# Optimization experiments

Hardware: AMD Instinct MI355X
Metric: run time of the kernel (lower is better)

## Reference

```python
import jax, jax.numpy as jnp
import numpy as np

N = 100000      # nodes
E = 3200000     # edges (avg degree 32)
DIN, DH, DOUT = 128, 32, 2


def setup_inputs() -> dict:
    key = jax.random.key(0)
    k1, k2, k3, k4 = jax.random.split(key, 4)
    x = jax.random.normal(k1, (N, DIN), dtype=jnp.float32)
    edge_index = jax.random.randint(k2, (2, E), 0, N, dtype=jnp.int64)
    # Glorot-ish scaled weights
    W1 = jax.random.normal(k3, (DIN, DH), dtype=jnp.float32) / np.sqrt(DIN)
    b1 = jnp.zeros((DH,), dtype=jnp.float32)
    W2 = jax.random.normal(k4, (DH, DOUT), dtype=jnp.float32) / np.sqrt(DH)
    b2 = jnp.zeros((DOUT,), dtype=jnp.float32)
    return {"x": x, "edge_index": edge_index, "W1": W1, "b1": b1, "W2": W2, "b2": b2}


def reference(x, edge_index, W1, b1, W2, b2):
    n = x.shape[0]
    # GCNConv default: add self-loops, symmetric deg^{-1/2} A deg^{-1/2} normalization
    loops = jnp.arange(n, dtype=edge_index.dtype)
    src = jnp.concatenate([edge_index[0], loops])  # [E+N]
    dst = jnp.concatenate([edge_index[1], loops])  # [E+N]
    deg = jax.ops.segment_sum(jnp.ones_like(dst, dtype=x.dtype), dst, num_segments=n)
    dinv = jnp.where(deg > 0, jax.lax.rsqrt(deg), 0.0)
    norm = dinv[src] * dinv[dst]  # [E+N]

    def gcn_layer(h, W, b):
        m = h @ W                                   # [n, dout] transform first (PyG order)
        msgs = m[src] * norm[:, None]               # gather + scale  [E+N, dout]
        agg = jax.ops.segment_sum(msgs, dst, num_segments=n)  # scatter-add
        return agg + b

    h = jax.nn.relu(gcn_layer(x, W1, b1))
    return gcn_layer(h, W2, b2)
```

## Files before the change

### kernel.cpp

```cpp
#include <hip/hip_runtime.h>
#include <hip/hip_bf16.h>

#define DIN 128
#define DH 32
#define DOUT 2
#define NPB 128
#define NPB_SHIFT 7
#define NBUK_MAX 1024
#define FILL_EDGES 8192

#define FXS1 262144.0f
#define FXI1 (1.0f / 262144.0f)
#define FXS2 131072.0f
#define FXI2 (1.0f / 131072.0f)


__device__ inline unsigned short f2bf(float f) {
    unsigned int u = __float_as_uint(f);
    u = (u + 0x7FFFu + ((u >> 16) & 1u)) >> 16;
    return (unsigned short)u;
}
__device__ inline float bfLO(unsigned int w) { return __uint_as_float(w << 16); }
__device__ inline float bfHI(unsigned int w) { return __uint_as_float(w & 0xFFFF0000u); }

__global__ void zero_gcnt_kernel(int* __restrict__ gcnt, int nbuk) {
    int i = blockIdx.x * blockDim.x + threadIdx.x;
    if (i < nbuk) gcnt[i] = 0;
}

__global__ void bukhist_kernel(const int* __restrict__ dst, int* __restrict__ gcnt,
                               int e, int nbuk) {
    __shared__ int lcnt[NBUK_MAX];
    int t = threadIdx.x;
    for (int i = t; i < nbuk; i += 256) lcnt[i] = 0;
    __syncthreads();
    int e0 = blockIdx.x * FILL_EDGES;
    int m = min(FILL_EDGES, e - e0);
    for (int i = t; i < m; i += 256) atomicAdd(&lcnt[dst[e0 + i] >> NPB_SHIFT], 1);
    __syncthreads();
    for (int i = t; i < nbuk; i += 256)
        if (lcnt[i]) atomicAdd(&gcnt[i], lcnt[i]);
}

__global__ void scan_kernel(const int* __restrict__ gcnt, int* __restrict__ gbase,
                            int* __restrict__ gcur, int nbuk,
                            unsigned short* __restrict__ mqc, int n) {
    __shared__ int sd[256];
    int t = threadIdx.x;
    if (t < 16) ((unsigned int*)(mqc + (size_t)n * DH))[t] = 0u;
    int v[4], s = 0;
#pragma unroll
    for (int k = 0; k < 4; ++k) {
        int i = 4 * t + k;
        v[k] = (i < nbuk) ? gcnt[i] : 0;
        s += v[k];
    }
    sd[t] = s;
    __syncthreads();
    for (int off = 1; off < 256; off <<= 1) {
        int x = (t >= off) ? sd[t - off] : 0;
        __syncthreads();
        sd[t] += x;
        __syncthreads();
    }
    int run = sd[t] - s;
#pragma unroll
    for (int k = 0; k < 4; ++k) {
        int i = 4 * t + k;
        if (i < nbuk) { gbase[i] = run; gcur[i] = run; }
        run += v[k];
    }
}

__global__ void binfill_kernel(const int* __restrict__ src, const int* __restrict__ dst,
                               int* __restrict__ gcur, unsigned int* __restrict__ binned,
                               int e, int nbuk) {
    __shared__ int cnt[NBUK_MAX];
    __shared__ int pos[NBUK_MAX];
    __shared__ int gb[NBUK_MAX];
    __shared__ unsigned int sorted[FILL_EDGES];
    __shared__ unsigned short aux[FILL_EDGES];
    __shared__ int stmp[256];

    int t = threadIdx.x;
    int e0 = blockIdx.x * FILL_EDGES;
    int m = min(FILL_EDGES, e - e0);

    for (int i = t; i < nbuk; i += 256) cnt[i] = 0;
    __syncthreads();
    for (int i = t; i < m; i += 256) atomicAdd(&cnt[dst[e0 + i] >> NPB_SHIFT], 1);
    __syncthreads();

    int v[4], s = 0;
#pragma unroll
    for (int k = 0; k < 4; ++k) {
        int i = 4 * t + k;
        v[k] = (i < nbuk) ? cnt[i] : 0;
        s += v[k];
    }
    stmp[t] = s;
    __syncthreads();
    for (int off = 1; off < 256; off <<= 1) {
        int x = (t >= off) ? stmp[t - off] : 0;
        __syncthreads();
        stmp[t] += x;
        __syncthreads();
    }
    int run = stmp[t] - s;
#pragma unroll
    for (int k = 0; k < 4; ++k) {
        int i = 4 * t + k;
        if (i < nbuk) pos[i] = run;
        run += v[k];
    }
    __syncthreads();

    for (int i = t; i < m; i += 256) {
        int d = dst[e0 + i];
        int sv = src[e0 + i];
        int b = d >> NPB_SHIFT;
        int r = atomicAdd(&pos[b], 1);
        sorted[r] = ((unsigned int)(d & (NPB - 1)) << 17) | (unsigned int)sv;
        aux[r] = (unsigned short)b;
    }
    __syncthreads();

    for (int b = t; b < nbuk; b += 256) {
        int c = cnt[b];
        gb[b] = c ? atomicAdd(&gcur[b], c) : 0;
    }
    __syncthreads();

    for (int i = t; i < m; i += 256) {
        int b = aux[i];
        int start = pos[b] - cnt[b];
        binned[gb[b] + (i - start)] = sorted[i];
    }
}

__global__ void bdinv_kernel(const int* __restrict__ gbase, const int* __restrict__ gcnt,
                             const unsigned int* __restrict__ binned,
                             float* __restrict__ dinv, int n) {
    __shared__ int cnt[NPB];
    int t = threadIdx.x;
    int b = blockIdx.x;
    if (t < NPB) cnt[t] = 0;
    __syncthreads();
    const int beg = gbase[b];
    const int cntb = gcnt[b];
    for (int i = t; i < cntb; i += 256) atomicAdd(&cnt[binned[beg + i] >> 17], 1);
    __syncthreads();
    if (t < NPB) {
        int r = (b << NPB_SHIFT) + t;
        if (r < n) dinv[r] = rsqrtf((float)(cnt[t] + 1));
    }
}

#define XLD 132
__global__ void gemm1_kernel(const float* __restrict__ x, const float* __restrict__ W1,
                             const float* __restrict__ dinv,
                             unsigned short* __restrict__ mqc, int n) {
    __shared__ float  Xl[32 * XLD];
    __shared__ float4 Wl4[DIN * 8];

    int t = threadIdx.x;
    for (int i = t; i < DIN * 8; i += 256) Wl4[i] = ((const float4*)W1)[i];

    int rb = blockIdx.x * 32;
    for (int i = t; i < 32 * 32; i += 256) {
        int rr = i >> 5, c4 = i & 31;
        int gr = rb + rr;
        float4 v = make_float4(0.f, 0.f, 0.f, 0.f);
        if (gr < n) v = ((const float4*)x)[(size_t)gr * 32 + c4];
        ((float4*)Xl)[rr * 33 + c4] = v;
    }
    __syncthreads();

    const int lane = t & 7;
    const int row  = t >> 3;
    const float* xrow = &Xl[row * XLD];
    float4 acc = make_float4(0.f, 0.f, 0.f, 0.f);
#pragma unroll
    for (int k = 0; k < DIN; ++k) {
        float xv = xrow[k];
        float4 w = Wl4[k * 8 + lane];
        acc.x += xv * w.x; acc.y += xv * w.y;
        acc.z += xv * w.z; acc.w += xv * w.w;
    }
    int r = rb + row;
    if (r < n) {
        float di = dinv[r];
        ushort4 sv;
        sv.x = f2bf(acc.x * di); sv.y = f2bf(acc.y * di);
        sv.z = f2bf(acc.z * di); sv.w = f2bf(acc.w * di);
        *(ushort4*)&mqc[(size_t)r * DH + 4 * lane] = sv;
    }
}

__global__ void __launch_bounds__(256, 4)
agg1_kernel(const int* __restrict__ gbase, const int* __restrict__ gcnt,
            const unsigned int* __restrict__ binned,
            const unsigned short* __restrict__ mqc,
            const float* __restrict__ dinv,
            const float* __restrict__ b1, const float* __restrict__ W2,
            float2* __restrict__ m2q, int n) {
    __shared__ int acc[NPB * 33];

    const int t = threadIdx.x;
    const int b = blockIdx.x;
    const int beg = gbase[b];
    const int cntb = gcnt[b];
    const int r0 = b << NPB_SHIFT;

    for (int i = t; i < NPB * 33; i += 256) acc[i] = 0;
    __syncthreads();

    const int g = t >> 4, l = t & 15;
    const unsigned int* __restrict__ bp = binned + beg;
    const unsigned int* __restrict__ mq32 = (const unsigned int*)mqc;

    int i = g;
    for (; i + 48 < cntb; i += 64) {
        unsigned int e0 = __builtin_nontemporal_load(&bp[i]);
        unsigned int e1 = __builtin_nontemporal_load(&bp[i + 16]);
        unsigned int e2 = __builtin_nontemporal_load(&bp[i + 32]);
        unsigned int e3 = __builtin_nontemporal_load(&bp[i + 48]);
        unsigned int w0 = mq32[(e0 & 0x1FFFFu) * 16u + l];
        unsigned int w1 = mq32[(e1 & 0x1FFFFu) * 16u + l];
        unsigned int w2 = mq32[(e2 & 0x1FFFFu) * 16u + l];
        unsigned int w3 = mq32[(e3 & 0x1FFFFu) * 16u + l];
        int d0 = (int)(e0 >> 17) * 33 + 2 * l;
        int d1 = (int)(e1 >> 17) * 33 + 2 * l;
        int d2 = (int)(e2 >> 17) * 33 + 2 * l;
        int d3 = (int)(e3 >> 17) * 33 + 2 * l;
        atomicAdd(&acc[d0], __float2int_rn(bfLO(w0) * FXS1));
        atomicAdd(&acc[d0 + 1], __float2int_rn(bfHI(w0) * FXS1));
        atomicAdd(&acc[d1], __float2int_rn(bfLO(w1) * FXS1));
        atomicAdd(&acc[d1 + 1], __float2int_rn(bfHI(w1) * FXS1));
        atomicAdd(&acc[d2], __float2int_rn(bfLO(w2) * FXS1));
        atomicAdd(&acc[d2 + 1], __float2int_rn(bfHI(w2) * FXS1));
        atomicAdd(&acc[d3], __float2int_rn(bfLO(w3) * FXS1));
        atomicAdd(&acc[d3 + 1], __float2int_rn(bfHI(w3) * FXS1));
    }
    for (; i < cntb; i += 16) {
        unsigned int e0 = __builtin_nontemporal_load(&bp[i]);
        unsigned int w0 = mq32[(e0 & 0x1FFFFu) * 16u + l];
        int d0 = (int)(e0 >> 17) * 33 + 2 * l;
        atomicAdd(&acc[d0], __float2int_rn(bfLO(w0) * FXS1));
        atomicAdd(&acc[d0 + 1], __float2int_rn(bfHI(w0) * FXS1));
    }
    __syncthreads();

    const int j = t >> 1, hf = t & 1;
    const int r = r0 + j;
    if (r < n) {
        const float di = dinv[r];
        const unsigned int* srow = mq32 + (size_t)r * 16 + hf * 8;
        const int* ar = &acc[j * 33 + hf * 16];
        float p0 = 0.f, p1 = 0.f;
#pragma unroll
        for (int k = 0; k < 8; ++k) {
            unsigned int sw = srow[k];
            int c = hf * 16 + 2 * k;
            float a0 = (float)ar[2 * k]     * FXI1;
            float a1 = (float)ar[2 * k + 1] * FXI1;
            float h0 = fmaxf(di * (a0 + bfLO(sw)) + b1[c],     0.0f);
            float h1 = fmaxf(di * (a1 + bfHI(sw)) + b1[c + 1], 0.0f);
            p0 += h0 * W2[2 * c]     + h1 * W2[2 * c + 2];
            p1 += h0 * W2[2 * c + 1] + h1 * W2[2 * c + 3];
        }
        p0 += __shfl_down(p0, 1, 2);
        p1 += __shfl_down(p1, 1, 2);
        if (hf == 0) m2q[r] = make_float2(di * p0, di * p1);
    }
}

__global__ void __launch_bounds__(256, 4)
agg2_kernel(const int* __restrict__ gbase, const int* __restrict__ gcnt,
            const unsigned int* __restrict__ binned,
            const float2* __restrict__ m2q,
            const float* __restrict__ dinv, const float* __restrict__ b2,
            float* __restrict__ out, int n) {
    __shared__ int a0s[NPB], a1s[NPB];
    const int t = threadIdx.x;
    const int b = blockIdx.x;
    const int beg = gbase[b];
    const int cntb = gcnt[b];
    const int r0 = b << NPB_SHIFT;

    if (t < NPB) { a0s[t] = 0; a1s[t] = 0; }
    __syncthreads();

    const unsigned int* __restrict__ bp = binned + beg;
    int i = t;
    for (; i + 768 < cntb; i += 1024) {
        unsigned int e0 = __builtin_nontemporal_load(&bp[i]);
        unsigned int e1 = __builtin_nontemporal_load(&bp[i + 256]);
        unsigned int e2 = __builtin_nontemporal_load(&bp[i + 512]);
        unsigned int e3 = __builtin_nontemporal_load(&bp[i + 768]);
        float2 v0 = m2q[e0 & 0x1FFFFu];
        float2 v1 = m2q[e1 & 0x1FFFFu];
        float2 v2 = m2q[e2 & 0x1FFFFu];
        float2 v3 = m2q[e3 & 0x1FFFFu];
        atomicAdd(&a0s[e0 >> 17], __float2int_rn(v0.x * FXS2));
        atomicAdd(&a1s[e0 >> 17], __float2int_rn(v0.y * FXS2));
        atomicAdd(&a0s[e1 >> 17], __float2int_rn(v1.x * FXS2));
        atomicAdd(&a1s[e1 >> 17], __float2int_rn(v1.y * FXS2));
        atomicAdd(&a0s[e2 >> 17], __float2int_rn(v2.x * FXS2));
        atomicAdd(&a1s[e2 >> 17], __float2int_rn(v2.y * FXS2));
        atomicAdd(&a0s[e3 >> 17], __float2int_rn(v3.x * FXS2));
        atomicAdd(&a1s[e3 >> 17], __float2int_rn(v3.y * FXS2));
    }
    for (; i < cntb; i += 256) {
        unsigned int e0 = __builtin_nontemporal_load(&bp[i]);
        float2 v0 = m2q[e0 & 0x1FFFFu];
        atomicAdd(&a0s[e0 >> 17], __float2int_rn(v0.x * FXS2));
        atomicAdd(&a1s[e0 >> 17], __float2int_rn(v0.y * FXS2));
    }
    __syncthreads();

    if (t < NPB) {
        int r = r0 + t;
        if (r < n) {
            float di = dinv[r];
            float2 self = m2q[r];
            out[(size_t)r * DOUT + 0] = di * ((float)a0s[t] * FXI2 + self.x) + b2[0];
            out[(size_t)r * DOUT + 1] = di * ((float)a1s[t] * FXI2 + self.y) + b2[1];
        }
    }
}

extern "C" void kernel_launch(void* const* d_in, const int* in_sizes, int n_in,
                              void* d_out, int out_size, void* d_ws, size_t ws_size,
                              hipStream_t stream) {
    const float* x  = (const float*)d_in[0];
    const int*   ei = (const int*)d_in[1];
    const float* W1 = (const float*)d_in[2];
    const float* b1 = (const float*)d_in[3];
    const float* W2 = (const float*)d_in[4];
    const float* b2 = (const float*)d_in[5];
    float* out = (float*)d_out;

    const int n = in_sizes[0] / DIN;
    const int e = in_sizes[1] / 2;
    const int* src = ei;
    const int* dst = ei + e;
    const int nbuk = (n + NPB - 1) >> NPB_SHIFT;

    char* ws = (char*)d_ws;
    float* dinv   = (float*)ws;          ws += (size_t)n * 4;
    int* gcnt     = (int*)ws;            ws += NBUK_MAX * 4;
    int* gbase    = (int*)ws;            ws += NBUK_MAX * 4;
    int* gcur     = (int*)ws;            ws += NBUK_MAX * 4;
    unsigned int* binned = (unsigned int*)ws;   ws += (size_t)e * 4;
    unsigned short* mqc  = (unsigned short*)ws; ws += ((size_t)n + 1) * DH * 2;
    float2* m2q   = (float2*)ws;

    const int B = 256;
    const int fill_blocks = (e + FILL_EDGES - 1) / FILL_EDGES;

    zero_gcnt_kernel<<<(nbuk + B - 1) / B, B, 0, stream>>>(gcnt, nbuk);
    bukhist_kernel<<<fill_blocks, B, 0, stream>>>(dst, gcnt, e, nbuk);
    scan_kernel<<<1, B, 0, stream>>>(gcnt, gbase, gcur, nbuk, mqc, n);
    binfill_kernel<<<fill_blocks, B, 0, stream>>>(src, dst, gcur, binned, e, nbuk);
    bdinv_kernel<<<nbuk, B, 0, stream>>>(gbase, gcnt, binned, dinv, n);
    gemm1_kernel<<<(n + 31) / 32, B, 0, stream>>>(x, W1, dinv, mqc, n);
    agg1_kernel<<<nbuk, B, 0, stream>>>(gbase, gcnt, binned, mqc, dinv, b1, W2, m2q, n);
    agg2_kernel<<<nbuk, B, 0, stream>>>(gbase, gcnt, binned, m2q, dinv, b2, out, n);
}
```

Before: 259.0 us.

## Double-buffer edge chunks in LDS and widen agg1 to 512 threads

agg1 now runs with 512 threads per block. Edge indices are streamed in 2048-entry chunks through a double-buffered LDS staging area, so the next chunk's global loads overlap with the gather and atomic work on the current one. The inner loop is unrolled to 8 gathers per thread to raise memory-level parallelism. The cost is more LDS per block, two barriers per chunk and sentinel padding work on partial chunks (sentinel index n points at the extra zeroed mqc row). Occupancy may also fall.

New measurement: 242.7 us. 1.07x faster.

```diff
diff --git a/kernel.cpp b/kernel.cpp
--- a/kernel.cpp
+++ b/kernel.cpp
@@ -8,6 +8,7 @@
 #define NPB_SHIFT 7
 #define NBUK_MAX 1024
 #define FILL_EDGES 8192
+#define ECHUNK 2048
 
 #define FXS1 262144.0f
 #define FXI1 (1.0f / 262144.0f)
@@ -197,7 +198,7 @@
     }
 }
 
-__global__ void __launch_bounds__(256, 4)
+__global__ void __launch_bounds__(512, 8)
 agg1_kernel(const int* __restrict__ gbase, const int* __restrict__ gcnt,
             const unsigned int* __restrict__ binned,
             const unsigned short* __restrict__ mqc,
@@ -205,6 +206,7 @@
             const float* __restrict__ b1, const float* __restrict__ W2,
             float2* __restrict__ m2q, int n) {
     __shared__ int acc[NPB * 33];
+    __shared__ unsigned int ebuf[2][ECHUNK];
 
     const int t = threadIdx.x;
     const int b = blockIdx.x;
@@ -212,56 +214,93 @@
     const int cntb = gcnt[b];
     const int r0 = b << NPB_SHIFT;
 
-    for (int i = t; i < NPB * 33; i += 256) acc[i] = 0;
-    __syncthreads();
-
-    const int g = t >> 4, l = t & 15;
+    for (int i = t; i < NPB * 33; i += 512) acc[i] = 0;
+
     const unsigned int* __restrict__ bp = binned + beg;
     const unsigned int* __restrict__ mq32 = (const unsigned int*)mqc;
-
-    int i = g;
-    for (; i + 48 < cntb; i += 64) {
-        unsigned int e0 = __builtin_nontemporal_load(&bp[i]);
-        unsigned int e1 = __builtin_nontemporal_load(&bp[i + 16]);
-        unsigned int e2 = __builtin_nontemporal_load(&bp[i + 32]);
-        unsigned int e3 = __builtin_nontemporal_load(&bp[i + 48]);
-        unsigned int w0 = mq32[(e0 & 0x1FFFFu) * 16u + l];
-        unsigned int w1 = mq32[(e1 & 0x1FFFFu) * 16u + l];
-        unsigned int w2 = mq32[(e2 & 0x1FFFFu) * 16u + l];
-        unsigned int w3 = mq32[(e3 & 0x1FFFFu) * 16u + l];
-        int d0 = (int)(e0 >> 17) * 33 + 2 * l;
-        int d1 = (int)(e1 >> 17) * 33 + 2 * l;
-        int d2 = (int)(e2 >> 17) * 33 + 2 * l;
-        int d3 = (int)(e3 >> 17) * 33 + 2 * l;
-        atomicAdd(&acc[d0], __float2int_rn(bfLO(w0) * FXS1));
-        atomicAdd(&acc[d0 + 1], __float2int_rn(bfHI(w0) * FXS1));
-        atomicAdd(&acc[d1], __float2int_rn(bfLO(w1) * FXS1));
-        atomicAdd(&acc[d1 + 1], __float2int_rn(bfHI(w1) * FXS1));
-        atomicAdd(&acc[d2], __float2int_rn(bfLO(w2) * FXS1));
-        atomicAdd(&acc[d2 + 1], __float2int_rn(bfHI(w2) * FXS1));
-        atomicAdd(&acc[d3], __float2int_rn(bfLO(w3) * FXS1));
-        atomicAdd(&acc[d3 + 1], __float2int_rn(bfHI(w3) * FXS1));
-    }
-    for (; i < cntb; i += 16) {
-        unsigned int e0 = __builtin_nontemporal_load(&bp[i]);
-        unsigned int w0 = mq32[(e0 & 0x1FFFFu) * 16u + l];
-        int d0 = (int)(e0 >> 17) * 33 + 2 * l;
-        atomicAdd(&acc[d0], __float2int_rn(bfLO(w0) * FXS1));
-        atomicAdd(&acc[d0 + 1], __float2int_rn(bfHI(w0) * FXS1));
-    }
-    __syncthreads();
-
-    const int j = t >> 1, hf = t & 1;
+    const unsigned int sent = (unsigned int)n;
+    const int nchunks = (cntb + ECHUNK - 1) / ECHUNK;
+
+    unsigned int st[4];
+    if (nchunks > 0) {
+#pragma unroll
+        for (int k = 0; k < 4; ++k) {
+            int idx = t + k * 512;
+            st[k] = (idx < cntb) ? __builtin_nontemporal_load(&bp[idx]) : sent;
+        }
+#pragma unroll
+        for (int k = 0; k < 4; ++k) ebuf[0][t + k * 512] = st[k];
+    }
+    __syncthreads();
+
+    const int g = t >> 4, l = t & 15;
+
+    for (int c = 0; c < nchunks; ++c) {
+        if (c + 1 < nchunks) {
+            const int base = (c + 1) * ECHUNK;
+#pragma unroll
+            for (int k = 0; k < 4; ++k) {
+                int idx = base + t + k * 512;
+                st[k] = (idx < cntb) ? __builtin_nontemporal_load(&bp[idx]) : sent;
+            }
+        }
+        const unsigned int* eb = ebuf[c & 1];
+        for (int j = 0; j < 64; j += 8) {
+            const unsigned int* ej = &eb[g + 32 * j];
+            unsigned int e0 = ej[0],   e1 = ej[32],  e2 = ej[64],  e3 = ej[96];
+            unsigned int e4 = ej[128], e5 = ej[160], e6 = ej[192], e7 = ej[224];
+            unsigned int w0 = mq32[(e0 & 0x1FFFFu) * 16u + l];
+            unsigned int w1 = mq32[(e1 & 0x1FFFFu) * 16u + l];
+            unsigned int w2 = mq32[(e2 & 0x1FFFFu) * 16u + l];
+            unsigned int w3 = mq32[(e3 & 0x1FFFFu) * 16u + l];
+            unsigned int w4 = mq32[(e4 & 0x1FFFFu) * 16u + l];
+            unsigned int w5 = mq32[(e5 & 0x1FFFFu) * 16u + l];
+            unsigned int w6 = mq32[(e6 & 0x1FFFFu) * 16u + l];
+            unsigned int w7 = mq32[(e7 & 0x1FFFFu) * 16u + l];
+            int d0 = (int)(e0 >> 17) * 33 + 2 * l;
+            int d1 = (int)(e1 >> 17) * 33 + 2 * l;
+            int d2 = (int)(e2 >> 17) * 33 + 2 * l;
+            int d3 = (int)(e3 >> 17) * 33 + 2 * l;
+            int d4 = (int)(e4 >> 17) * 33 + 2 * l;
+            int d5 = (int)(e5 >> 17) * 33 + 2 * l;
+            int d6 = (int)(e6 >> 17) * 33 + 2 * l;
+            int d7 = (int)(e7 >> 17) * 33 + 2 * l;
+            atomicAdd(&acc[d0], __float2int_rn(bfLO(w0) * FXS1));
+            atomicAdd(&acc[d0 + 1], __float2int_rn(bfHI(w0) * FXS1));
+            atomicAdd(&acc[d1], __float2int_rn(bfLO(w1) * FXS1));
+            atomicAdd(&acc[d1 + 1], __float2int_rn(bfHI(w1) * FXS1));
+            atomicAdd(&acc[d2], __float2int_rn(bfLO(w2) * FXS1));
+            atomicAdd(&acc[d2 + 1], __float2int_rn(bfHI(w2) * FXS1));
+            atomicAdd(&acc[d3], __float2int_rn(bfLO(w3) * FXS1));
+            atomicAdd(&acc[d3 + 1], __float2int_rn(bfHI(w3) * FXS1));
+            atomicAdd(&acc[d4], __float2int_rn(bfLO(w4) * FXS1));
+            atomicAdd(&acc[d4 + 1], __float2int_rn(bfHI(w4) * FXS1));
+            atomicAdd(&acc[d5], __float2int_rn(bfLO(w5) * FXS1));
+            atomicAdd(&acc[d5 + 1], __float2int_rn(bfHI(w5) * FXS1));
+            atomicAdd(&acc[d6], __float2int_rn(bfLO(w6) * FXS1));
+            atomicAdd(&acc[d6 + 1], __float2int_rn(bfHI(w6) * FXS1));
+            atomicAdd(&acc[d7], __float2int_rn(bfLO(w7) * FXS1));
+            atomicAdd(&acc[d7 + 1], __float2int_rn(bfHI(w7) * FXS1));
+        }
+        __syncthreads();
+        if (c + 1 < nchunks) {
+#pragma unroll
+            for (int k = 0; k < 4; ++k) ebuf[(c + 1) & 1][t + k * 512] = st[k];
+        }
+        __syncthreads();
+    }
+
+    const int j = t >> 2, q = t & 3;
     const int r = r0 + j;
     if (r < n) {
         const float di = dinv[r];
-        const unsigned int* srow = mq32 + (size_t)r * 16 + hf * 8;
-        const int* ar = &acc[j * 33 + hf * 16];
+        const unsigned int* srow = mq32 + (size_t)r * 16 + q * 4;
+        const int* ar = &acc[j * 33 + q * 8];
         float p0 = 0.f, p1 = 0.f;
 #pragma unroll
-        for (int k = 0; k < 8; ++k) {
+        for (int k = 0; k < 4; ++k) {
             unsigned int sw = srow[k];
-            int c = hf * 16 + 2 * k;
+            int c = q * 8 + 2 * k;
             float a0 = (float)ar[2 * k]     * FXI1;
             float a1 = (float)ar[2 * k + 1] * FXI1;
             float h0 = fmaxf(di * (a0 + bfLO(sw)) + b1[c],     0.0f);
@@ -269,9 +308,9 @@
             p0 += h0 * W2[2 * c]     + h1 * W2[2 * c + 2];
             p1 += h0 * W2[2 * c + 1] + h1 * W2[2 * c + 3];
         }
-        p0 += __shfl_down(p0, 1, 2);
-        p1 += __shfl_down(p1, 1, 2);
-        if (hf == 0) m2q[r] = make_float2(di * p0, di * p1);
+        p0 += __shfl_down(p0, 2, 4); p0 += __shfl_down(p0, 1, 4);
+        p1 += __shfl_down(p1, 2, 4); p1 += __shfl_down(p1, 1, 4);
+        if (q == 0) m2q[r] = make_float2(di * p0, di * p1);
     }
 }
 
@@ -365,6 +404,6 @@
     binfill_kernel<<<fill_blocks, B, 0, stream>>>(src, dst, gcur, binned, e, nbuk);
     bdinv_kernel<<<nbuk, B, 0, stream>>>(gbase, gcnt, binned, dinv, n);
     gemm1_kernel<<<(n + 31) / 32, B, 0, stream>>>(x, W1, dinv, mqc, n);
-    agg1_kernel<<<nbuk, B, 0, stream>>>(gbase, gcnt, binned, mqc, dinv, b1, W2, m2q, n);
+    agg1_kernel<<<nbuk, 512, 0, stream>>>(gbase, gcnt, binned, mqc, dinv, b1, W2, m2q, n);
     agg2_kernel<<<nbuk, B, 0, stream>>>(gbase, gcnt, binned, m2q, dinv, b2, out, n);
 }
```
